# Optimization experiments

Measured on AMD Instinct MI355X. Metric: run time of the kernel, lower is better.

The kernel has to match this reference:

```python
import jax, jax.numpy as jnp
import numpy as np

B, N, C = 2, 4096, 1024
H, WIN = 16, 20
D = C // H

def setup_inputs() -> dict:
    key = jax.random.key(0)
    ks = jax.random.split(key, 9)
    s = 1.0 / np.sqrt(C)
    d = {"q": jax.random.normal(ks[0], (B, N, C), jnp.float32)}
    for i, name in enumerate(["Wq", "Wk", "Wv", "Wo"]):
        d[name + "_w"] = jax.random.normal(ks[1 + 2 * i], (C, C), jnp.float32) * s
        d[name + "_b"] = jax.random.normal(ks[2 + 2 * i], (C,), jnp.float32) * 0.01
    return d

def reference(q, Wq_w, Wq_b, Wk_w, Wk_b, Wv_w, Wv_b, Wo_w, Wo_b):
    b, n, c = q.shape
    w2 = WIN // 2  # half window = 10
    def proj(x, w, bias):
        return (x @ w.T + bias).reshape(b, n, H, D).transpose(0, 2, 1, 3)  # [B,H,N,D]
    Q = proj(q, Wq_w, Wq_b)
    K = proj(q, Wk_w, Wk_b)
    V = proj(q, Wv_w, Wv_b)
    off = jnp.arange(-w2, w2 + 1)                       # [Wn] = 21 offsets
    pos = jnp.arange(n)[:, None] + off[None, :]         # [N, Wn] key index per query
    valid = (pos >= 0) & (pos < n)                      # edge clipping == torch start/end slicing
    idx = jnp.clip(pos, 0, n - 1)
    Kw = K[:, :, idx, :]                                # [B,H,N,Wn,D] gathered key windows
    Vw = V[:, :, idx, :]
    scale = jnp.sqrt(jnp.float32(D))
    scores = jnp.einsum('bhnd,bhnwd->bhnw', Q, Kw) / scale
    scores = jnp.where(valid[None, None], scores, -jnp.inf)
    probs = jax.nn.softmax(scores, axis=-1)             # invalid slots get exactly 0
    out = jnp.einsum('bhnw,bhnwd->bhnd', probs, Vw)
    out = out.transpose(0, 2, 1, 3).reshape(b, n, c)
    out = out @ Wo_w.T + Wo_b
    # torch returns attn_probs of the LAST loop iteration i=N-1: window [N-1-w2, N), size w2+1
    attn_last = probs[:, :, -1:, : w2 + 1]              # [B,H,1,11]
    return (out, attn_last)
```

## Files before the change

### kernel.cpp

```cpp
#include <hip/hip_runtime.h>
#include <hip/hip_bf16.h>

#define Bb 2
#define Nn 4096
#define Cc 1024
#define Hh 16
#define Dd 64
#define Mm (Bb*Nn)
#define W2 10
#define WINSZ 21

typedef __attribute__((ext_vector_type(8))) short  bf16x8s;
typedef __attribute__((ext_vector_type(4))) float  f32x4;
typedef __attribute__((ext_vector_type(4))) unsigned short us4;

#define AS1 __attribute__((address_space(1)))
#define AS3 __attribute__((address_space(3)))

__device__ __forceinline__ unsigned short f2bf(float f) {
  unsigned int u = __float_as_uint(f);
  u += 0x7FFFu + ((u >> 16) & 1u);
  return (unsigned short)(u >> 16);
}
__device__ __forceinline__ float bflo(unsigned int u) { return __uint_as_float(u << 16); }
__device__ __forceinline__ float bfhi(unsigned int u) { return __uint_as_float(u & 0xFFFF0000u); }

__device__ __forceinline__ us4 cvt4(float4 v) {
  us4 o;
  o.x = f2bf(v.x); o.y = f2bf(v.y); o.z = f2bf(v.z); o.w = f2bf(v.w);
  return o;
}

__global__ __launch_bounds__(256) void cvt_all(const float4* __restrict__ q,
                                               const float4* __restrict__ wq,
                                               const float4* __restrict__ wk,
                                               const float4* __restrict__ wv,
                                               const float4* __restrict__ wo,
                                               const float* __restrict__ bq,
                                               const float* __restrict__ bk,
                                               const float* __restrict__ bv,
                                               us4* __restrict__ qb4,
                                               us4* __restrict__ wqkv4,
                                               us4* __restrict__ wo4,
                                               float* __restrict__ bqkv) {
  const int NQ = 2097152, NW = 262144, TOT = NQ + 4 * NW;
  const int gid = blockIdx.x * 256 + threadIdx.x;
  const int stride = gridDim.x * 256;
  for (int i = gid; i < TOT; i += stride) {
    if (i < NQ) {
      qb4[i] = cvt4(q[i]);
    } else {
      int j = i - NQ;
      int r = j >> 18, k = j & (NW - 1);
      if (r == 0)      wqkv4[k]          = cvt4(wq[k]);
      else if (r == 1) wqkv4[NW + k]     = cvt4(wk[k]);
      else if (r == 2) wqkv4[2 * NW + k] = cvt4(wv[k]);
      else             wo4[k]            = cvt4(wo[k]);
    }
  }
  if (gid < 3072) {
    float v = (gid < 1024) ? bq[gid] : (gid < 2048) ? bk[gid - 1024] : bv[gid - 2048];
    bqkv[gid] = v;
  }
}

template<bool OUT_BF16>
__global__ __launch_bounds__(512) void gemm_p3(const unsigned short* __restrict__ A,
                                               const unsigned short* __restrict__ Bm,
                                               const float* __restrict__ bias,
                                               void* __restrict__ Cout,
                                               int N) {
  constexpr int K = 1024, NT = 16, NBM = Mm / 128;
  __shared__ unsigned short lds[3][24576];

  const int tid = threadIdx.x, wid = tid >> 6, lane = tid & 63;
  const int wm = wid >> 2, wn = wid & 3;

  const int nwg = gridDim.x, cpx = nwg >> 3, bid = blockIdx.x;
  const int swz = (bid & 7) * cpx + (bid >> 3);
  const int m0 = (swz % NBM) << 7, n0 = (swz / NBM) << 8;

  const int rbase = wid * 8 + (lane >> 3);
  const int cst = ((lane & 7) ^ (lane >> 3)) * 8;
  const unsigned short* aS0 = A + (size_t)(m0 + rbase) * K + cst;
  const unsigned short* aS1 = A + (size_t)(m0 + 64 + rbase) * K + cst;
  const unsigned short* bS0 = Bm + (size_t)(n0 + rbase) * K + cst;
  const unsigned short* bS1 = Bm + (size_t)(n0 + 64 + rbase) * K + cst;
  const unsigned short* bS2 = Bm + (size_t)(n0 + 128 + rbase) * K + cst;
  const unsigned short* bS3 = Bm + (size_t)(n0 + 192 + rbase) * K + cst;
  const int dA0 = wid * 512, dA1 = 4096 + wid * 512;
  const int dB0 = 8192 + wid * 512, dB1 = 12288 + wid * 512;
  const int dB2 = 16384 + wid * 512, dB3 = 20480 + wid * 512;

#define STG(bf, kt) do {                                                                   \
    const size_t ko = (size_t)(kt) * 64;                                                   \
    __builtin_amdgcn_global_load_lds((AS1 const void*)(aS0 + ko), (AS3 void*)(&lds[bf][dA0]), 16, 0, 0); \
    __builtin_amdgcn_global_load_lds((AS1 const void*)(aS1 + ko), (AS3 void*)(&lds[bf][dA1]), 16, 0, 0); \
    __builtin_amdgcn_global_load_lds((AS1 const void*)(bS0 + ko), (AS3 void*)(&lds[bf][dB0]), 16, 0, 0); \
    __builtin_amdgcn_global_load_lds((AS1 const void*)(bS1 + ko), (AS3 void*)(&lds[bf][dB1]), 16, 0, 0); \
    __builtin_amdgcn_global_load_lds((AS1 const void*)(bS2 + ko), (AS3 void*)(&lds[bf][dB2]), 16, 0, 0); \
    __builtin_amdgcn_global_load_lds((AS1 const void*)(bS3 + ko), (AS3 void*)(&lds[bf][dB3]), 16, 0, 0); \
  } while (0)

  int aoff[2][4], boff[2][4];
#pragma unroll
  for (int kk = 0; kk < 2; ++kk) {
    const int chs = ((kk * 4 + (lane >> 4)) ^ (lane & 7)) * 8;
#pragma unroll
    for (int f = 0; f < 4; ++f) {
      aoff[kk][f] = (wm * 64 + f * 16 + (lane & 15)) * 64 + chs;
      boff[kk][f] = 8192 + (wn * 64 + f * 16 + (lane & 15)) * 64 + chs;
    }
  }

  f32x4 acc[4][4] = {};

  STG(0, 0);
  STG(1, 1);
  asm volatile("s_waitcnt vmcnt(6)" ::: "memory");
  __builtin_amdgcn_sched_barrier(0);
  __builtin_amdgcn_s_barrier();
  __builtin_amdgcn_sched_barrier(0);

  int cur = 0, stg = 2;
  for (int t = 0; t < NT; ++t) {
    if (t + 2 < NT) STG(stg, t + 2);

    const unsigned short* L = &lds[cur][0];
    bf16x8s a[2][4], b[2][4];
#pragma unroll
    for (int kk = 0; kk < 2; ++kk) {
#pragma unroll
      for (int f = 0; f < 4; ++f) {
        a[kk][f] = *(const bf16x8s*)(L + aoff[kk][f]);
        b[kk][f] = *(const bf16x8s*)(L + boff[kk][f]);
      }
    }
    __builtin_amdgcn_s_setprio(1);
#pragma unroll
    for (int kk = 0; kk < 2; ++kk)
#pragma unroll
      for (int fm = 0; fm < 4; ++fm)
#pragma unroll
        for (int fn = 0; fn < 4; ++fn)
          acc[fm][fn] = __builtin_amdgcn_mfma_f32_16x16x32_bf16(a[kk][fm], b[kk][fn], acc[fm][fn], 0, 0, 0);
    __builtin_amdgcn_s_setprio(0);

    if (t + 1 < NT) {
      if (t + 2 < NT) asm volatile("s_waitcnt vmcnt(6)" ::: "memory");
      else            asm volatile("s_waitcnt vmcnt(0)" ::: "memory");
      __builtin_amdgcn_sched_barrier(0);
      __builtin_amdgcn_s_barrier();
      __builtin_amdgcn_sched_barrier(0);
    }
    cur = (cur == 2) ? 0 : cur + 1;
    stg = (stg == 2) ? 0 : stg + 1;
  }
#undef STG

  const int r0 = m0 + wm * 64 + (lane >> 4) * 4;
  const int c0 = n0 + wn * 64 + (lane & 15);
#pragma unroll
  for (int fm = 0; fm < 4; ++fm) {
#pragma unroll
    for (int fn = 0; fn < 4; ++fn) {
      const int col = c0 + fn * 16;
      const float bv = bias[col];
#pragma unroll
      for (int r = 0; r < 4; ++r) {
        const int row = r0 + fm * 16 + r;
        const float v = acc[fm][fn][r] + bv;
        if (OUT_BF16)
          ((unsigned short*)Cout)[(size_t)row * N + col] = f2bf(v);
        else
          ((float*)Cout)[(size_t)row * N + col] = v;
      }
    }
  }
}

#define TN 128
#define KVROWS (TN + 2 * W2)

__global__ void attn_kernel(const unsigned short* __restrict__ QKV,
                            unsigned short* __restrict__ AO,
                            float* __restrict__ attn_last) {
  __shared__ uint4 Kl[KVROWS * 8];
  __shared__ uint4 Vl[KVROWS * 8];

  const int nt = Nn / TN;
  const int bid = blockIdx.x;
  const int tile = bid & (nt - 1);
  const int bh = bid / nt;
  const int h = bh & (Hh - 1), b = bh / Hh;
  const int n0 = tile * TN;
  const int tid = threadIdx.x;

  for (int idx = tid; idx < KVROWS * 8; idx += 256) {
    const int r = idx >> 3, c = idx & 7;
    const int pos = n0 - W2 + r;
    uint4 kv = make_uint4(0, 0, 0, 0), vv = make_uint4(0, 0, 0, 0);
    if (pos >= 0 && pos < Nn) {
      const uint4* row = (const uint4*)(QKV + (size_t)(b * Nn + pos) * 3072);
      kv = row[128 + h * 8 + c];
      vv = row[256 + h * 8 + c];
    }
    const int slot = c ^ (r & 7);
    Kl[r * 8 + slot] = kv;
    Vl[r * 8 + slot] = vv;
  }
  __syncthreads();

  const int row  = tid >> 1;
  const int half = tid & 1;
  const int n = n0 + row;
  const size_t m = (size_t)b * Nn + n;

  const uint4* qrow = (const uint4*)(QKV + m * 3072) + h * 8 + half * 4;
  const uint4 qd0 = qrow[0], qd1 = qrow[1], qd2 = qrow[2], qd3 = qrow[3];

  float p[WINSZ];
#pragma unroll
  for (int w = 0; w < WINSZ; ++w) p[w] = 0.f;

#pragma unroll
  for (int c = 0; c < 4; ++c) {
    const uint4 qv = (c == 0) ? qd0 : (c == 1) ? qd1 : (c == 2) ? qd2 : qd3;
    const float q0 = bflo(qv.x), q1 = bfhi(qv.x);
    const float q2 = bflo(qv.y), q3 = bfhi(qv.y);
    const float q4 = bflo(qv.z), q5 = bfhi(qv.z);
    const float q6 = bflo(qv.w), q7 = bfhi(qv.w);
#pragma unroll 7
    for (int w = 0; w < WINSZ; ++w) {
      const int r = row + w;
      const uint4 v = Kl[r * 8 + ((half * 4 + c) ^ (r & 7))];
      float a0 = q0 * bflo(v.x);
      float a1 = q1 * bfhi(v.x);
      a0 += q2 * bflo(v.y);
      a1 += q3 * bfhi(v.y);
      a0 += q4 * bflo(v.z);
      a1 += q5 * bfhi(v.z);
      a0 += q6 * bflo(v.w);
      a1 += q7 * bfhi(v.w);
      p[w] += a0 + a1;
    }
  }

#pragma unroll
  for (int w = 0; w < WINSZ; ++w) {
    float t = p[w];
    t += __shfl_xor(t, 1, 64);
    const int pos = n - W2 + w;
    p[w] = (pos < 0 || pos >= Nn) ? -1e30f : t * 0.125f;
  }
  float mx = p[0];
#pragma unroll
  for (int w = 1; w < WINSZ; ++w) mx = fmaxf(mx, p[w]);
  float sum = 0.f;
#pragma unroll
  for (int w = 0; w < WINSZ; ++w) { p[w] = __expf(p[w] - mx); sum += p[w]; }
  const float inv = 1.0f / sum;

  if (n == Nn - 1 && half == 0) {
#pragma unroll
    for (int w = 0; w <= W2; ++w)
      attn_last[(b * Hh + h) * (W2 + 1) + w] = p[w] * inv;
  }

  uint4* orow = (uint4*)(AO + m * Cc + h * Dd) + half * 4;
#pragma unroll
  for (int c = 0; c < 4; ++c) {
    float o0 = 0.f, o1 = 0.f, o2 = 0.f, o3 = 0.f;
    float o4 = 0.f, o5 = 0.f, o6 = 0.f, o7 = 0.f;
#pragma unroll 7
    for (int w = 0; w < WINSZ; ++w) {
      const int r = row + w;
      const uint4 v = Vl[r * 8 + ((half * 4 + c) ^ (r & 7))];
      const float pw = p[w];
      o0 += pw * bflo(v.x);
      o1 += pw * bfhi(v.x);
      o2 += pw * bflo(v.y);
      o3 += pw * bfhi(v.y);
      o4 += pw * bflo(v.z);
      o5 += pw * bfhi(v.z);
      o6 += pw * bflo(v.w);
      o7 += pw * bfhi(v.w);
    }
    unsigned int d0 = (unsigned int)f2bf(o0 * inv) | ((unsigned int)f2bf(o1 * inv) << 16);
    unsigned int d1 = (unsigned int)f2bf(o2 * inv) | ((unsigned int)f2bf(o3 * inv) << 16);
    unsigned int d2 = (unsigned int)f2bf(o4 * inv) | ((unsigned int)f2bf(o5 * inv) << 16);
    unsigned int d3 = (unsigned int)f2bf(o6 * inv) | ((unsigned int)f2bf(o7 * inv) << 16);
    orow[c] = make_uint4(d0, d1, d2, d3);
  }
}

extern "C" void kernel_launch(void* const* d_in, const int* in_sizes, int n_in,
                              void* d_out, int out_size, void* d_ws, size_t ws_size,
                              hipStream_t stream) {
  const float* q    = (const float*)d_in[0];
  const float* Wq_w = (const float*)d_in[1];
  const float* Wq_b = (const float*)d_in[2];
  const float* Wk_w = (const float*)d_in[3];
  const float* Wk_b = (const float*)d_in[4];
  const float* Wv_w = (const float*)d_in[5];
  const float* Wv_b = (const float*)d_in[6];
  const float* Wo_w = (const float*)d_in[7];
  const float* Wo_b = (const float*)d_in[8];
  float* out = (float*)d_out;
  float* attn_last = out + (size_t)Mm * Cc;

  char* ws = (char*)d_ws;
  unsigned short* qb   = (unsigned short*)(ws);
  unsigned short* Wqkv = (unsigned short*)(ws + 16777216);
  unsigned short* Wo16 = (unsigned short*)(ws + 16777216 + 6291456);
  float*          bqkv = (float*)(ws + 25165824);
  unsigned short* QKV  = (unsigned short*)(ws + 25182208);
  unsigned short* AO   = (unsigned short*)(ws + 75513856);

  cvt_all<<<2048, 256, 0, stream>>>((const float4*)q,
                                    (const float4*)Wq_w, (const float4*)Wk_w,
                                    (const float4*)Wv_w, (const float4*)Wo_w,
                                    Wq_b, Wk_b, Wv_b,
                                    (us4*)qb, (us4*)Wqkv, (us4*)Wo16, bqkv);

  {
    dim3 grid((Mm / 128) * (3072 / 256));
    gemm_p3<true><<<grid, 512, 0, stream>>>(qb, Wqkv, bqkv, (void*)QKV, 3072);
  }

  {
    dim3 grid(Bb * Hh * (Nn / TN));
    attn_kernel<<<grid, 256, 0, stream>>>(QKV, AO, attn_last);
  }

  {
    dim3 grid((Mm / 128) * (Cc / 256));
    gemm_p3<false><<<grid, 512, 0, stream>>>(AO, Wo16, Wo_b, (void*)out, Cc);
  }
}
```

Measured before the change: 134.5 us.

## Switch GEMMs to 128x128 tiles with 4 waves and double buffering

Replaces the 128x256 tile GEMM, which used 8 waves and a triple-buffered LDS pipeline, with a 128x128 tile GEMM using 4 waves in a 2x2 layout and a double-buffered LDS pipeline. Each wave still computes a 64x64 sub-tile. LDS per block drops from 144KB to 64KB, which allows more blocks per CU, and the grid doubles, which helps the smaller output-projection GEMM fill the GPU. In exchange there is less operand reuse per block and a shallower prefetch, since each iteration now waits for all outstanding loads before the barrier.

```diff
diff --git a/kernel.cpp b/kernel.cpp
--- a/kernel.cpp
+++ b/kernel.cpp
@@ -65,41 +65,44 @@
 }
 
 template<bool OUT_BF16>
-__global__ __launch_bounds__(512) void gemm_p3(const unsigned short* __restrict__ A,
+__global__ __launch_bounds__(256) void gemm_22(const unsigned short* __restrict__ A,
                                                const unsigned short* __restrict__ Bm,
                                                const float* __restrict__ bias,
                                                void* __restrict__ Cout,
                                                int N) {
-  constexpr int K = 1024, NT = 16, NBM = Mm / 128;
-  __shared__ unsigned short lds[3][24576];
+  constexpr int K = 1024, NT = 16;
+  __shared__ unsigned short lds[2][16384];
 
   const int tid = threadIdx.x, wid = tid >> 6, lane = tid & 63;
-  const int wm = wid >> 2, wn = wid & 3;
+  const int wm = wid >> 1, wn = wid & 1;
 
   const int nwg = gridDim.x, cpx = nwg >> 3, bid = blockIdx.x;
   const int swz = (bid & 7) * cpx + (bid >> 3);
-  const int m0 = (swz % NBM) << 7, n0 = (swz / NBM) << 8;
-
-  const int rbase = wid * 8 + (lane >> 3);
+  constexpr int NBM = Mm / 128;
+  const int m0 = (swz % NBM) << 7, n0 = (swz / NBM) << 7;
+
+  const int srow = lane >> 3;
   const int cst = ((lane & 7) ^ (lane >> 3)) * 8;
-  const unsigned short* aS0 = A + (size_t)(m0 + rbase) * K + cst;
-  const unsigned short* aS1 = A + (size_t)(m0 + 64 + rbase) * K + cst;
-  const unsigned short* bS0 = Bm + (size_t)(n0 + rbase) * K + cst;
-  const unsigned short* bS1 = Bm + (size_t)(n0 + 64 + rbase) * K + cst;
-  const unsigned short* bS2 = Bm + (size_t)(n0 + 128 + rbase) * K + cst;
-  const unsigned short* bS3 = Bm + (size_t)(n0 + 192 + rbase) * K + cst;
-  const int dA0 = wid * 512, dA1 = 4096 + wid * 512;
-  const int dB0 = 8192 + wid * 512, dB1 = 12288 + wid * 512;
-  const int dB2 = 16384 + wid * 512, dB3 = 20480 + wid * 512;
-
-#define STG(bf, kt) do {                                                                   \
-    const size_t ko = (size_t)(kt) * 64;                                                   \
-    __builtin_amdgcn_global_load_lds((AS1 const void*)(aS0 + ko), (AS3 void*)(&lds[bf][dA0]), 16, 0, 0); \
-    __builtin_amdgcn_global_load_lds((AS1 const void*)(aS1 + ko), (AS3 void*)(&lds[bf][dA1]), 16, 0, 0); \
-    __builtin_amdgcn_global_load_lds((AS1 const void*)(bS0 + ko), (AS3 void*)(&lds[bf][dB0]), 16, 0, 0); \
-    __builtin_amdgcn_global_load_lds((AS1 const void*)(bS1 + ko), (AS3 void*)(&lds[bf][dB1]), 16, 0, 0); \
-    __builtin_amdgcn_global_load_lds((AS1 const void*)(bS2 + ko), (AS3 void*)(&lds[bf][dB2]), 16, 0, 0); \
-    __builtin_amdgcn_global_load_lds((AS1 const void*)(bS3 + ko), (AS3 void*)(&lds[bf][dB3]), 16, 0, 0); \
+  const unsigned short* aS[4];
+  const unsigned short* bS[4];
+#pragma unroll
+  for (int j = 0; j < 4; ++j) {
+    aS[j] = A  + (size_t)(m0 + wid * 32 + j * 8 + srow) * K + cst;
+    bS[j] = Bm + (size_t)(n0 + wid * 32 + j * 8 + srow) * K + cst;
+  }
+  const int dA = wid * 2048;
+  const int dB = 8192 + wid * 2048;
+
+#define STG(bf, kt) do {                                                                     \
+    const size_t ko = (size_t)(kt) * 64;                                                     \
+    __builtin_amdgcn_global_load_lds((AS1 const void*)(aS[0] + ko), (AS3 void*)(&lds[bf][dA       ]), 16, 0, 0); \
+    __builtin_amdgcn_global_load_lds((AS1 const void*)(aS[1] + ko), (AS3 void*)(&lds[bf][dA +  512]), 16, 0, 0); \
+    __builtin_amdgcn_global_load_lds((AS1 const void*)(aS[2] + ko), (AS3 void*)(&lds[bf][dA + 1024]), 16, 0, 0); \
+    __builtin_amdgcn_global_load_lds((AS1 const void*)(aS[3] + ko), (AS3 void*)(&lds[bf][dA + 1536]), 16, 0, 0); \
+    __builtin_amdgcn_global_load_lds((AS1 const void*)(bS[0] + ko), (AS3 void*)(&lds[bf][dB       ]), 16, 0, 0); \
+    __builtin_amdgcn_global_load_lds((AS1 const void*)(bS[1] + ko), (AS3 void*)(&lds[bf][dB +  512]), 16, 0, 0); \
+    __builtin_amdgcn_global_load_lds((AS1 const void*)(bS[2] + ko), (AS3 void*)(&lds[bf][dB + 1024]), 16, 0, 0); \
+    __builtin_amdgcn_global_load_lds((AS1 const void*)(bS[3] + ko), (AS3 void*)(&lds[bf][dB + 1536]), 16, 0, 0); \
   } while (0)
 
   int aoff[2][4], boff[2][4];
@@ -116,26 +119,26 @@
   f32x4 acc[4][4] = {};
 
   STG(0, 0);
-  STG(1, 1);
-  asm volatile("s_waitcnt vmcnt(6)" ::: "memory");
+  asm volatile("s_waitcnt vmcnt(0)" ::: "memory");
   __builtin_amdgcn_sched_barrier(0);
   __builtin_amdgcn_s_barrier();
   __builtin_amdgcn_sched_barrier(0);
 
-  int cur = 0, stg = 2;
+  int cur = 0;
+#pragma unroll 1
   for (int t = 0; t < NT; ++t) {
-    if (t + 2 < NT) STG(stg, t + 2);
+    if (t + 1 < NT) STG(cur ^ 1, t + 1);
 
     const unsigned short* L = &lds[cur][0];
     bf16x8s a[2][4], b[2][4];
 #pragma unroll
-    for (int kk = 0; kk < 2; ++kk) {
+    for (int kk = 0; kk < 2; ++kk)
 #pragma unroll
       for (int f = 0; f < 4; ++f) {
         a[kk][f] = *(const bf16x8s*)(L + aoff[kk][f]);
         b[kk][f] = *(const bf16x8s*)(L + boff[kk][f]);
       }
-    }
+
     __builtin_amdgcn_s_setprio(1);
 #pragma unroll
     for (int kk = 0; kk < 2; ++kk)
@@ -147,14 +150,12 @@
     __builtin_amdgcn_s_setprio(0);
 
     if (t + 1 < NT) {
-      if (t + 2 < NT) asm volatile("s_waitcnt vmcnt(6)" ::: "memory");
-      else            asm volatile("s_waitcnt vmcnt(0)" ::: "memory");
+      asm volatile("s_waitcnt vmcnt(0)" ::: "memory");
       __builtin_amdgcn_sched_barrier(0);
       __builtin_amdgcn_s_barrier();
       __builtin_amdgcn_sched_barrier(0);
     }
-    cur = (cur == 2) ? 0 : cur + 1;
-    stg = (stg == 2) ? 0 : stg + 1;
+    cur ^= 1;
   }
 #undef STG
 
@@ -324,8 +325,8 @@
                                     (us4*)qb, (us4*)Wqkv, (us4*)Wo16, bqkv);
 
   {
-    dim3 grid((Mm / 128) * (3072 / 256));
-    gemm_p3<true><<<grid, 512, 0, stream>>>(qb, Wqkv, bqkv, (void*)QKV, 3072);
+    dim3 grid((Mm / 128) * (3072 / 128));
+    gemm_22<true><<<grid, 256, 0, stream>>>(qb, Wqkv, bqkv, (void*)QKV, 3072);
   }
 
   {
@@ -334,7 +335,7 @@
   }
 
   {
-    dim3 grid((Mm / 128) * (Cc / 256));
-    gemm_p3<false><<<grid, 512, 0, stream>>>(AO, Wo16, Wo_b, (void*)out, Cc);
-  }
-}
+    dim3 grid((Mm / 128) * (Cc / 128));
+    gemm_22<false><<<grid, 256, 0, stream>>>(AO, Wo16, Wo_b, (void*)out, Cc);
+  }
+}
```

New measurement: 147.3 us. 1.09x slower.
